# Kernel optimization log

Hardware: AMD Instinct MI355X
Metric: run time of the kernel (lower is better)

## Reference

```python
import jax, jax.numpy as jnp
import numpy as np

N_HEAD = 12

def setup_inputs() -> dict:
    key = jax.random.key(0)
    k1, k2, k3 = jax.random.split(key, 3)
    B, T, C = 2, 4096, 768
    x = jax.random.normal(k1, (B, T, C), dtype=jnp.float32)
    Wqkv = jax.random.normal(k2, (C, 3 * C), dtype=jnp.float32) * (1.0 / np.sqrt(C))
    bqkv = jnp.zeros((3 * C,), dtype=jnp.float32)
    Wout = jax.random.normal(k3, (C, C), dtype=jnp.float32) * (1.0 / np.sqrt(C))
    bout = jnp.zeros((C,), dtype=jnp.float32)
    return {"x": x, "Wqkv": Wqkv, "bqkv": bqkv, "Wout": Wout, "bout": bout}

def reference(x, Wqkv, bqkv, Wout, bout):
    B, T, C = x.shape
    H = N_HEAD
    D = C // H
    qkv = x @ Wqkv + bqkv                       # [B,T,3C]
    qkv = qkv.reshape(B, T, 3, H, D)
    q = qkv[:, :, 0].transpose(0, 2, 1, 3)       # [B,H,T,D]
    k = qkv[:, :, 1].transpose(0, 2, 1, 3)
    v = qkv[:, :, 2].transpose(0, 2, 1, 3)
    att = jnp.einsum('bhqd,bhkd->bhqk', q, k) / jnp.sqrt(jnp.float32(D))
    causal = jnp.tril(jnp.ones((T, T), dtype=bool))
    att = jnp.where(causal[None, None], att, jnp.float32(-jnp.inf))
    att = jax.nn.softmax(att, axis=-1)
    out = jnp.einsum('bhqk,bhkd->bhqd', att, v)  # [B,H,T,D]
    out = out.transpose(0, 2, 1, 3).reshape(B, T, C)
    return out @ Wout + bout
```

## Files before the change

### kernel.cpp

```cpp
#include <hip/hip_runtime.h>
#include <math.h>

#define Bb 2
#define Tt 4096
#define Cc 768
#define Hh 12
#define Dd 64

typedef __attribute__((ext_vector_type(8))) short short8;
typedef __attribute__((ext_vector_type(4))) float f32x4;
typedef __attribute__((ext_vector_type(4))) unsigned short u16x4;

static __device__ __forceinline__ unsigned short f2bf(float f) {
    unsigned u = __float_as_uint(f);
    u += 0x7FFF + ((u >> 16) & 1);
    return (unsigned short)(u >> 16);
}

static __device__ __forceinline__ float ex2(float x) {
    return __builtin_amdgcn_exp2f(x);
}

static __device__ __forceinline__ void gload16(const void* g, void* l) {
    __builtin_amdgcn_global_load_lds(
        (const __attribute__((address_space(1))) unsigned*)g,
        (__attribute__((address_space(3))) unsigned*)l, 16, 0, 0);
}

__global__ __launch_bounds__(256)
void cvt_bf16(const float* __restrict__ in, unsigned short* __restrict__ out, int n8) {
    int i = blockIdx.x * 256 + threadIdx.x;
    if (i >= n8) return;
    float4 a = *(const float4*)(in + (size_t)i * 8);
    float4 b = *(const float4*)(in + (size_t)i * 8 + 4);
    union { short8 v; unsigned short u[8]; } p;
    p.u[0] = f2bf(a.x); p.u[1] = f2bf(a.y); p.u[2] = f2bf(a.z); p.u[3] = f2bf(a.w);
    p.u[4] = f2bf(b.x); p.u[5] = f2bf(b.y); p.u[6] = f2bf(b.z); p.u[7] = f2bf(b.w);
    *(short8*)(out + (size_t)i * 8) = p.v;
}

__global__ __launch_bounds__(256)
void transpose_w(const float* __restrict__ W, unsigned short* __restrict__ Wt,
                 int K, int N) {
    __shared__ __align__(16) unsigned short Tl[64][72];
    int n0 = blockIdx.x * 64, k0 = blockIdx.y * 64;
    int t = threadIdx.x;
    int r = t >> 2, c = (t & 3) * 16;
    const float* wp = W + (size_t)(k0 + r) * N + n0 + c;
    #pragma unroll
    for (int j = 0; j < 16; j += 4) {
        float4 v = *(const float4*)(wp + j);
        Tl[c + j + 0][r] = f2bf(v.x);
        Tl[c + j + 1][r] = f2bf(v.y);
        Tl[c + j + 2][r] = f2bf(v.z);
        Tl[c + j + 3][r] = f2bf(v.w);
    }
    __syncthreads();
    unsigned short* op = Wt + (size_t)(n0 + r) * K + k0 + c;
    *(short8*)op       = *(const short8*)&Tl[r][c];
    *(short8*)(op + 8) = *(const short8*)&Tl[r][c + 8];
}

template<bool BF16OUT>
__global__ __launch_bounds__(256)
void gemm_mfma(const unsigned short* __restrict__ A, const unsigned short* __restrict__ Bt,
               const float* __restrict__ bias, void* __restrict__ Cout,
               int M, int N, int K, int qcols,
               unsigned short* __restrict__ vtb, int voff) {
    union SmemU {
        unsigned short ab[2][128][64];
        unsigned short tv[128][136];
    };
    __shared__ __align__(16) SmemU sh;
    const int tid = threadIdx.x;
    const int wid = tid >> 6, lane = tid & 63;
    const int lr = lane & 15, g = lane >> 4;
    const int wr = wid >> 1, wc = wid & 1;
    const int m0 = blockIdx.y * 128, n0 = blockIdx.x * 128;
    const int srow = lane >> 3;
    const int scol = (lane & 7) * 8;

    f32x4 acc[4][4] = {};

    for (int k0 = 0; k0 < K; k0 += 64) {
        #pragma unroll
        for (int j = 0; j < 4; ++j) {
            int ci = wid * 4 + j;
            int row = ci * 8 + srow;
            gload16(A  + (size_t)(m0 + row) * K + k0 + scol, &sh.ab[0][ci * 8][0]);
            gload16(Bt + (size_t)(n0 + row) * K + k0 + scol, &sh.ab[1][ci * 8][0]);
        }
        __syncthreads();
        #pragma unroll
        for (int ks = 0; ks < 2; ++ks) {
            short8 af[4], bfr[4];
            #pragma unroll
            for (int m = 0; m < 4; ++m)
                af[m] = *(const short8*)&sh.ab[0][wr * 64 + m * 16 + lr][ks * 32 + g * 8];
            #pragma unroll
            for (int n = 0; n < 4; ++n)
                bfr[n] = *(const short8*)&sh.ab[1][wc * 64 + n * 16 + lr][ks * 32 + g * 8];
            #pragma unroll
            for (int m = 0; m < 4; ++m)
                #pragma unroll
                for (int n = 0; n < 4; ++n)
                    acc[m][n] = __builtin_amdgcn_mfma_f32_16x16x32_bf16(
                        af[m], bfr[n], acc[m][n], 0, 0, 0);
        }
        __syncthreads();
    }

    if (vtb != nullptr && n0 >= voff) {
        #pragma unroll
        for (int n = 0; n < 4; ++n) {
            int tcol = wc * 64 + n * 16 + lr;
            float bv = bias[n0 + tcol];
            #pragma unroll
            for (int m = 0; m < 4; ++m) {
                int trow = wr * 64 + m * 16 + g * 4;
                #pragma unroll
                for (int r = 0; r < 4; ++r)
                    sh.tv[tcol][trow + r] = f2bf(acc[m][n][r] + bv);
            }
        }
        __syncthreads();
        const int dlocal = tid >> 1;
        const int th     = (tid & 1) * 64;
        const int colg   = n0 + dlocal;
        const int hd     = (colg - voff) >> 6;
        const int d      = (colg - voff) & 63;
        const int token  = m0 + th;
        const int bq     = token >> 12;
        const int t0     = token & (Tt - 1);
        unsigned short* dst = vtb + ((size_t)(bq * Hh + hd) * Dd + d) * Tt + t0;
        const unsigned short* src = &sh.tv[dlocal][th];
        #pragma unroll
        for (int j = 0; j < 8; ++j)
            *(short8*)(dst + j * 8) = *(const short8*)(src + j * 8);
        return;
    }

    const float qscale = 0.125f * 1.44269504088896340736f;
    #pragma unroll
    for (int n = 0; n < 4; ++n) {
        int coln = n0 + wc * 64 + n * 16 + lr;
        float bv = bias[coln];
        float sc = (coln < qcols) ? qscale : 1.0f;
        #pragma unroll
        for (int m = 0; m < 4; ++m) {
            int rowb = m0 + wr * 64 + m * 16 + g * 4;
            #pragma unroll
            for (int r = 0; r < 4; ++r) {
                float v = (acc[m][n][r] + bv) * sc;
                if (BF16OUT)
                    ((unsigned short*)Cout)[(size_t)(rowb + r) * N + coln] = f2bf(v);
                else
                    ((float*)Cout)[(size_t)(rowb + r) * N + coln] = v;
            }
        }
    }
}

__global__ __launch_bounds__(512)
void attn_mfma(const unsigned short* __restrict__ qkvb,
               const unsigned short* __restrict__ vtb,
               unsigned short* __restrict__ outb) {
    const int nid  = blockIdx.x;
    const int xcd  = nid & 7;
    const int rest = nid >> 3;
    const int P    = rest & 31;
    const int H2   = xcd + 8 * (rest >> 5);
    const int hd   = H2 % Hh;
    const int b    = H2 / Hh;
    const int tid = threadIdx.x;
    const int wid = tid >> 6, lane = tid & 63;
    const int strip = wid & 3, kh = wid >> 2;
    const int lr = lane & 15, g = lane >> 4;
    const int rm7 = lr & 7;
    const size_t rs = 3 * Cc;

    __shared__ __align__(16) unsigned short Ks[2][64 * 64];
    __shared__ __align__(16) unsigned short Vs[2][64 * 64];
    __shared__ __align__(16) float combO[4][64][16];
    __shared__ float combL[4][64];

    const unsigned short* qkvbase = qkvb + (size_t)b * Tt * rs;
    const unsigned short* vbase   = vtb + (size_t)((b * Hh + hd) * Dd) * Tt;

    const int row0 = tid >> 3;
    const int slog = (tid & 7) ^ (row0 & 7);
    const unsigned short* ksrc0 = qkvbase + (size_t)row0 * rs + Cc + hd * Dd + slog * 8;
    const unsigned short* vsrc0 = vbase + (size_t)row0 * Tt + slog * 8;

    const int ntA = 64 - P;
    const int qA  = (63 - P) * 64 + strip * 16 + lr;
    const int qB  = P * 64 + strip * 16 + lr;

    short8 qfA0, qfA1, qfB0, qfB1;
    {
        const unsigned short* qp = qkvbase + (size_t)qA * rs + hd * Dd;
        qfA0 = *(const short8*)(qp + g * 8);
        qfA1 = *(const short8*)(qp + 32 + g * 8);
        qp = qkvbase + (size_t)qB * rs + hd * Dd;
        qfB0 = *(const short8*)(qp + g * 8);
        qfB1 = *(const short8*)(qp + 32 + g * 8);
    }

    auto stage = [&](int buf, int ts) {
        int t = (ts < ntA) ? ts : ts - ntA;
        gload16(ksrc0 + (size_t)t * 64 * rs, &Ks[buf][wid * 512]);
        gload16(vsrc0 + t * 64,              &Vs[buf][wid * 512]);
    };

    stage(0, 0);
    __syncthreads();
    int cur = 0;

    const int laneA = lr + ((g & 1) << 5);
    const int laneB = laneA + 16;
    const int asel  = g >> 1;

    f32x4 o[4];
    #pragma unroll
    for (int dt = 0; dt < 4; ++dt) o[dt] = (f32x4){0.f, 0.f, 0.f, 0.f};
    float lpart = 0.f;
    short8 qf0 = qfA0, qf1 = qfA1;
    int myq = qA;

    auto combine_epilogue = [&]() {
        if (kh) {
            #pragma unroll
            for (int dt = 0; dt < 4; ++dt)
                *(f32x4*)&combO[strip][lane][dt * 4] = o[dt];
            combL[strip][lane] = lpart;
        }
        __syncthreads();
        if (!kh) {
            float l_r = lpart + combL[strip][lane];
            l_r += __shfl_xor(l_r, 16);
            l_r += __shfl_xor(l_r, 32);
            float inv = 1.f / fmaxf(l_r, 1e-37f);
            unsigned short* op = outb + ((size_t)b * Tt + myq) * Cc + hd * Dd + g * 4;
            #pragma unroll
            for (int dt = 0; dt < 4; ++dt) {
                f32x4 t2 = *(const f32x4*)&combO[strip][lane][dt * 4];
                u16x4 w;
                #pragma unroll
                for (int r = 0; r < 4; ++r) w[r] = f2bf((o[dt][r] + t2[r]) * inv);
                *(u16x4*)(op + dt * 16) = w;
            }
        }
        __syncthreads();
    };

    #pragma unroll 1
    for (int ts = 0; ts < 65; ++ts) {
        if (ts + 1 < 65) stage(cur ^ 1, ts + 1);

        const int inA = (ts < ntA) ? 1 : 0;
        const int kbt = inA ? ts : ts - ntA;
        const int nt  = inA ? ntA : (65 - ntA);
        const unsigned short* Kc = &Ks[cur][0];
        const unsigned short* Vc = &Vs[cur][0];

        f32x4 st[2];
        __builtin_amdgcn_s_setprio(1);
        #pragma unroll
        for (int kt = 0; kt < 2; ++kt) {
            int row = kh * 32 + kt * 16 + lr;
            int off0 = row * 64 + (g ^ rm7) * 8;
            short8 kf0 = *(const short8*)&Kc[off0];
            short8 kf1 = *(const short8*)&Kc[off0 ^ 32];
            f32x4 a = (f32x4){0.f, 0.f, 0.f, 0.f};
            a = __builtin_amdgcn_mfma_f32_16x16x32_bf16(kf0, qf0, a, 0, 0, 0);
            a = __builtin_amdgcn_mfma_f32_16x16x32_bf16(kf1, qf1, a, 0, 0, 0);
            st[kt] = a;
        }
        __builtin_amdgcn_s_setprio(0);

        if (kbt == nt - 1) {
            #pragma unroll
            for (int kt = 0; kt < 2; ++kt)
                #pragma unroll
                for (int r = 0; r < 4; ++r)
                    if (kbt * 64 + kh * 32 + kt * 16 + g * 4 + r > myq)
                        st[kt][r] = -1e30f;
        }

        float psum = 0.f;
        #pragma unroll
        for (int kt = 0; kt < 2; ++kt)
            #pragma unroll
            for (int r = 0; r < 4; ++r) {
                float p = ex2(st[kt][r]);
                st[kt][r] = p;
                psum += p;
            }
        lpart += psum;

        unsigned up[2][2];
        #pragma unroll
        for (int kt = 0; kt < 2; ++kt) {
            asm("v_cvt_pk_bf16_f32 %0, %1, %2"
                : "=v"(up[kt][0]) : "v"(st[kt][0]), "v"(st[kt][1]));
            asm("v_cvt_pk_bf16_f32 %0, %1, %2"
                : "=v"(up[kt][1]) : "v"(st[kt][2]), "v"(st[kt][3]));
        }
        {
            unsigned wa0 = __shfl(up[0][0], laneA);
            unsigned wb0 = __shfl(up[1][0], laneA);
            unsigned wa1 = __shfl(up[0][1], laneA);
            unsigned wb1 = __shfl(up[1][1], laneA);
            unsigned wa2 = __shfl(up[0][0], laneB);
            unsigned wb2 = __shfl(up[1][0], laneB);
            unsigned wa3 = __shfl(up[0][1], laneB);
            unsigned wb3 = __shfl(up[1][1], laneB);
            union { unsigned w[4]; short8 v; } pb;
            pb.w[0] = asel ? wb0 : wa0;
            pb.w[1] = asel ? wb1 : wa1;
            pb.w[2] = asel ? wb2 : wa2;
            pb.w[3] = asel ? wb3 : wa3;
            __builtin_amdgcn_s_setprio(1);
            #pragma unroll
            for (int dt = 0; dt < 4; ++dt) {
                int row = dt * 16 + lr;
                int off = row * 64 + (((kh << 2) | g) ^ rm7) * 8;
                short8 vf = *(const short8*)&Vc[off];
                o[dt] = __builtin_amdgcn_mfma_f32_16x16x32_bf16(vf, pb.v, o[dt], 0, 0, 0);
            }
            __builtin_amdgcn_s_setprio(0);
        }

        __syncthreads();
        cur ^= 1;

        if (ts == ntA - 1) {
            combine_epilogue();
            #pragma unroll
            for (int dt = 0; dt < 4; ++dt) o[dt] = (f32x4){0.f, 0.f, 0.f, 0.f};
            lpart = 0.f;
            qf0 = qfB0; qf1 = qfB1;
            myq = qB;
        }
    }

    combine_epilogue();
}

extern "C" void kernel_launch(void* const* d_in, const int* in_sizes, int n_in,
                              void* d_out, int out_size, void* d_ws, size_t ws_size,
                              hipStream_t stream) {
    const float* x    = (const float*)d_in[0];
    const float* Wqkv = (const float*)d_in[1];
    const float* bqkv = (const float*)d_in[2];
    const float* Wout = (const float*)d_in[3];
    const float* bout = (const float*)d_in[4];
    float* out = (float*)d_out;

    const int M = Bb * Tt;
    const int N1 = 3 * Cc;

    char* p = (char*)d_ws;
    unsigned short* qkvb  = (unsigned short*)p; p += (size_t)M * N1 * 2;
    unsigned short* xb    = (unsigned short*)p; p += (size_t)M * Cc * 2;
    unsigned short* wqkvt = (unsigned short*)p; p += (size_t)N1 * Cc * 2;
    unsigned short* woutt = (unsigned short*)p; p += (size_t)Cc * Cc * 2;
    unsigned short* vtb   = (unsigned short*)p; p += (size_t)Bb * Hh * Dd * Tt * 2;
    unsigned short* attb  = (unsigned short*)p; p += (size_t)M * Cc * 2;

    cvt_bf16<<<dim3((M * Cc / 8 + 255) / 256), dim3(256), 0, stream>>>(x, xb, M * Cc / 8);
    transpose_w<<<dim3(N1 / 64, Cc / 64), dim3(256), 0, stream>>>(Wqkv, wqkvt, Cc, N1);
    transpose_w<<<dim3(Cc / 64, Cc / 64), dim3(256), 0, stream>>>(Wout, woutt, Cc, Cc);

    gemm_mfma<true><<<dim3(N1 / 128, M / 128), dim3(256), 0, stream>>>(
        xb, wqkvt, bqkv, qkvb, M, N1, Cc, Cc, vtb, 2 * Cc);

    attn_mfma<<<dim3(32 * Hh * Bb), dim3(512), 0, stream>>>(qkvb, vtb, attb);

    gemm_mfma<false><<<dim3(Cc / 128, M / 128), dim3(256), 0, stream>>>(
        attb, woutt, bout, out, M, Cc, Cc, 0, nullptr, 1 << 30);
}
```

Before: 194.2 us.

## Halve attention block to 4 waves, each handling two 16-row query sub-tiles

The attention kernel now runs 256 threads (4 waves) instead of 8. Each wave processes two 16-row query sub-tiles, so each K and V fragment read from LDS feeds two MFMAs. Each thread issues twice as many staging loads, and per-thread accumulator and register state roughly doubles. The intent is to halve LDS fragment traffic per unit of compute and cut barrier participants, at the cost of fewer waves for latency hiding and higher register pressure.

```diff
diff --git a/kernel.cpp b/kernel.cpp
--- a/kernel.cpp
+++ b/kernel.cpp
@@ -161,7 +161,7 @@
     }
 }
 
-__global__ __launch_bounds__(512)
+__global__ __launch_bounds__(256)
 void attn_mfma(const unsigned short* __restrict__ qkvb,
                const unsigned short* __restrict__ vtb,
                unsigned short* __restrict__ outb) {
@@ -174,42 +174,46 @@
     const int b    = H2 / Hh;
     const int tid = threadIdx.x;
     const int wid = tid >> 6, lane = tid & 63;
-    const int strip = wid & 3, kh = wid >> 2;
+    const int strip = wid & 1, kh = wid >> 1;
     const int lr = lane & 15, g = lane >> 4;
     const int rm7 = lr & 7;
     const size_t rs = 3 * Cc;
 
     __shared__ __align__(16) unsigned short Ks[2][64 * 64];
     __shared__ __align__(16) unsigned short Vs[2][64 * 64];
-    __shared__ __align__(16) float combO[4][64][16];
-    __shared__ float combL[4][64];
+    __shared__ __align__(16) float combO[2][2][64][16];
+    __shared__ float combL[2][2][64];
 
     const unsigned short* qkvbase = qkvb + (size_t)b * Tt * rs;
     const unsigned short* vbase   = vtb + (size_t)((b * Hh + hd) * Dd) * Tt;
 
-    const int row0 = tid >> 3;
-    const int slog = (tid & 7) ^ (row0 & 7);
+    const int srw  = lane >> 3;
+    const int row0 = wid * 8 + srw;
+    const int slog = (lane & 7) ^ (srw & 7);
     const unsigned short* ksrc0 = qkvbase + (size_t)row0 * rs + Cc + hd * Dd + slog * 8;
     const unsigned short* vsrc0 = vbase + (size_t)row0 * Tt + slog * 8;
 
     const int ntA = 64 - P;
-    const int qA  = (63 - P) * 64 + strip * 16 + lr;
-    const int qB  = P * 64 + strip * 16 + lr;
-
-    short8 qfA0, qfA1, qfB0, qfB1;
-    {
-        const unsigned short* qp = qkvbase + (size_t)qA * rs + hd * Dd;
-        qfA0 = *(const short8*)(qp + g * 8);
-        qfA1 = *(const short8*)(qp + 32 + g * 8);
-        qp = qkvbase + (size_t)qB * rs + hd * Dd;
-        qfB0 = *(const short8*)(qp + g * 8);
-        qfB1 = *(const short8*)(qp + 32 + g * 8);
+    const int qA0 = (63 - P) * 64 + strip * 32;
+    const int qB0 = P * 64 + strip * 32;
+
+    short8 qfA[2][2], qfB[2][2];
+    #pragma unroll
+    for (int sub = 0; sub < 2; ++sub) {
+        const unsigned short* qp = qkvbase + (size_t)(qA0 + sub * 16 + lr) * rs + hd * Dd;
+        qfA[sub][0] = *(const short8*)(qp + g * 8);
+        qfA[sub][1] = *(const short8*)(qp + 32 + g * 8);
+        qp = qkvbase + (size_t)(qB0 + sub * 16 + lr) * rs + hd * Dd;
+        qfB[sub][0] = *(const short8*)(qp + g * 8);
+        qfB[sub][1] = *(const short8*)(qp + 32 + g * 8);
     }
 
     auto stage = [&](int buf, int ts) {
         int t = (ts < ntA) ? ts : ts - ntA;
-        gload16(ksrc0 + (size_t)t * 64 * rs, &Ks[buf][wid * 512]);
-        gload16(vsrc0 + t * 64,              &Vs[buf][wid * 512]);
+        gload16(ksrc0 + (size_t)t * 64 * rs,        &Ks[buf][wid * 512]);
+        gload16(ksrc0 + (size_t)(t * 64 + 32) * rs, &Ks[buf][2048 + wid * 512]);
+        gload16(vsrc0 + t * 64,                     &Vs[buf][wid * 512]);
+        gload16(vsrc0 + (size_t)32 * Tt + t * 64,   &Vs[buf][2048 + wid * 512]);
     };
 
     stage(0, 0);
@@ -220,34 +224,48 @@
     const int laneB = laneA + 16;
     const int asel  = g >> 1;
 
-    f32x4 o[4];
+    f32x4 o[2][4];
     #pragma unroll
-    for (int dt = 0; dt < 4; ++dt) o[dt] = (f32x4){0.f, 0.f, 0.f, 0.f};
-    float lpart = 0.f;
-    short8 qf0 = qfA0, qf1 = qfA1;
-    int myq = qA;
+    for (int sub = 0; sub < 2; ++sub)
+        #pragma unroll
+        for (int dt = 0; dt < 4; ++dt) o[sub][dt] = (f32x4){0.f, 0.f, 0.f, 0.f};
+    float lpart[2] = {0.f, 0.f};
+    short8 qf[2][2];
+    #pragma unroll
+    for (int sub = 0; sub < 2; ++sub) {
+        qf[sub][0] = qfA[sub][0]; qf[sub][1] = qfA[sub][1];
+    }
+    int myq0 = qA0 + lr;
 
     auto combine_epilogue = [&]() {
         if (kh) {
             #pragma unroll
-            for (int dt = 0; dt < 4; ++dt)
-                *(f32x4*)&combO[strip][lane][dt * 4] = o[dt];
-            combL[strip][lane] = lpart;
+            for (int sub = 0; sub < 2; ++sub) {
+                #pragma unroll
+                for (int dt = 0; dt < 4; ++dt)
+                    *(f32x4*)&combO[strip][sub][lane][dt * 4] = o[sub][dt];
+                combL[strip][sub][lane] = lpart[sub];
+            }
         }
         __syncthreads();
         if (!kh) {
-            float l_r = lpart + combL[strip][lane];
-            l_r += __shfl_xor(l_r, 16);
-            l_r += __shfl_xor(l_r, 32);
-            float inv = 1.f / fmaxf(l_r, 1e-37f);
-            unsigned short* op = outb + ((size_t)b * Tt + myq) * Cc + hd * Dd + g * 4;
-            #pragma unroll
-            for (int dt = 0; dt < 4; ++dt) {
-                f32x4 t2 = *(const f32x4*)&combO[strip][lane][dt * 4];
-                u16x4 w;
-                #pragma unroll
-                for (int r = 0; r < 4; ++r) w[r] = f2bf((o[dt][r] + t2[r]) * inv);
-                *(u16x4*)(op + dt * 16) = w;
+            #pragma unroll
+            for (int sub = 0; sub < 2; ++sub) {
+                float l_r = lpart[sub] + combL[strip][sub][lane];
+                l_r += __shfl_xor(l_r, 16);
+                l_r += __shfl_xor(l_r, 32);
+                float inv = 1.f / fmaxf(l_r, 1e-37f);
+                unsigned short* op = outb + ((size_t)b * Tt + myq0 + sub * 16) * Cc
+                                     + hd * Dd + g * 4;
+                #pragma unroll
+                for (int dt = 0; dt < 4; ++dt) {
+                    f32x4 t2 = *(const f32x4*)&combO[strip][sub][lane][dt * 4];
+                    u16x4 w;
+                    #pragma unroll
+                    for (int r = 0; r < 4; ++r)
+                        w[r] = f2bf((o[sub][dt][r] + t2[r]) * inv);
+                    *(u16x4*)(op + dt * 16) = w;
+                }
             }
         }
         __syncthreads();
@@ -263,50 +281,63 @@
         const unsigned short* Kc = &Ks[cur][0];
         const unsigned short* Vc = &Vs[cur][0];
 
-        f32x4 st[2];
+        f32x4 st[2][2];
         __builtin_amdgcn_s_setprio(1);
         #pragma unroll
         for (int kt = 0; kt < 2; ++kt) {
-            int row = kh * 32 + kt * 16 + lr;
-            int off0 = row * 64 + (g ^ rm7) * 8;
+            int krow = kh * 32 + kt * 16 + lr;
+            int off0 = krow * 64 + (g ^ rm7) * 8;
             short8 kf0 = *(const short8*)&Kc[off0];
             short8 kf1 = *(const short8*)&Kc[off0 ^ 32];
-            f32x4 a = (f32x4){0.f, 0.f, 0.f, 0.f};
-            a = __builtin_amdgcn_mfma_f32_16x16x32_bf16(kf0, qf0, a, 0, 0, 0);
-            a = __builtin_amdgcn_mfma_f32_16x16x32_bf16(kf1, qf1, a, 0, 0, 0);
-            st[kt] = a;
+            #pragma unroll
+            for (int sub = 0; sub < 2; ++sub) {
+                f32x4 a = (f32x4){0.f, 0.f, 0.f, 0.f};
+                a = __builtin_amdgcn_mfma_f32_16x16x32_bf16(kf0, qf[sub][0], a, 0, 0, 0);
+                a = __builtin_amdgcn_mfma_f32_16x16x32_bf16(kf1, qf[sub][1], a, 0, 0, 0);
+                st[sub][kt] = a;
+            }
         }
         __builtin_amdgcn_s_setprio(0);
 
+        short8 vf[4];
+        #pragma unroll
+        for (int dt = 0; dt < 4; ++dt) {
+            int off = (dt * 16 + lr) * 64 + (((kh << 2) | g) ^ rm7) * 8;
+            vf[dt] = *(const short8*)&Vc[off];
+        }
+
         if (kbt == nt - 1) {
             #pragma unroll
+            for (int sub = 0; sub < 2; ++sub)
+                #pragma unroll
+                for (int kt = 0; kt < 2; ++kt)
+                    #pragma unroll
+                    for (int r = 0; r < 4; ++r)
+                        if (kbt * 64 + kh * 32 + kt * 16 + g * 4 + r > myq0 + sub * 16)
+                            st[sub][kt][r] = -1e30f;
+        }
+
+        #pragma unroll
+        for (int sub = 0; sub < 2; ++sub) {
+            float psum = 0.f;
+            #pragma unroll
             for (int kt = 0; kt < 2; ++kt)
                 #pragma unroll
-                for (int r = 0; r < 4; ++r)
-                    if (kbt * 64 + kh * 32 + kt * 16 + g * 4 + r > myq)
-                        st[kt][r] = -1e30f;
-        }
-
-        float psum = 0.f;
-        #pragma unroll
-        for (int kt = 0; kt < 2; ++kt)
-            #pragma unroll
-            for (int r = 0; r < 4; ++r) {
-                float p = ex2(st[kt][r]);
-                st[kt][r] = p;
-                psum += p;
-            }
-        lpart += psum;
-
-        unsigned up[2][2];
-        #pragma unroll
-        for (int kt = 0; kt < 2; ++kt) {
-            asm("v_cvt_pk_bf16_f32 %0, %1, %2"
-                : "=v"(up[kt][0]) : "v"(st[kt][0]), "v"(st[kt][1]));
-            asm("v_cvt_pk_bf16_f32 %0, %1, %2"
-                : "=v"(up[kt][1]) : "v"(st[kt][2]), "v"(st[kt][3]));
-        }
-        {
+                for (int r = 0; r < 4; ++r) {
+                    float p = ex2(st[sub][kt][r]);
+                    st[sub][kt][r] = p;
+                    psum += p;
+                }
+            lpart[sub] += psum;
+
+            unsigned up[2][2];
+            #pragma unroll
+            for (int kt = 0; kt < 2; ++kt) {
+                asm("v_cvt_pk_bf16_f32 %0, %1, %2"
+                    : "=v"(up[kt][0]) : "v"(st[sub][kt][0]), "v"(st[sub][kt][1]));
+                asm("v_cvt_pk_bf16_f32 %0, %1, %2"
+                    : "=v"(up[kt][1]) : "v"(st[sub][kt][2]), "v"(st[sub][kt][3]));
+            }
             unsigned wa0 = __shfl(up[0][0], laneA);
             unsigned wb0 = __shfl(up[1][0], laneA);
             unsigned wa1 = __shfl(up[0][1], laneA);
@@ -322,12 +353,9 @@
             pb.w[3] = asel ? wb3 : wa3;
             __builtin_amdgcn_s_setprio(1);
             #pragma unroll
-            for (int dt = 0; dt < 4; ++dt) {
-                int row = dt * 16 + lr;
-                int off = row * 64 + (((kh << 2) | g) ^ rm7) * 8;
-                short8 vf = *(const short8*)&Vc[off];
-                o[dt] = __builtin_amdgcn_mfma_f32_16x16x32_bf16(vf, pb.v, o[dt], 0, 0, 0);
-            }
+            for (int dt = 0; dt < 4; ++dt)
+                o[sub][dt] = __builtin_amdgcn_mfma_f32_16x16x32_bf16(
+                    vf[dt], pb.v, o[sub][dt], 0, 0, 0);
             __builtin_amdgcn_s_setprio(0);
         }
 
@@ -337,10 +365,13 @@
         if (ts == ntA - 1) {
             combine_epilogue();
             #pragma unroll
-            for (int dt = 0; dt < 4; ++dt) o[dt] = (f32x4){0.f, 0.f, 0.f, 0.f};
-            lpart = 0.f;
-            qf0 = qfB0; qf1 = qfB1;
-            myq = qB;
+            for (int sub = 0; sub < 2; ++sub) {
+                #pragma unroll
+                for (int dt = 0; dt < 4; ++dt) o[sub][dt] = (f32x4){0.f, 0.f, 0.f, 0.f};
+                lpart[sub] = 0.f;
+                qf[sub][0] = qfB[sub][0]; qf[sub][1] = qfB[sub][1];
+            }
+            myq0 = qB0 + lr;
         }
     }
 
@@ -375,7 +406,7 @@
     gemm_mfma<true><<<dim3(N1 / 128, M / 128), dim3(256), 0, stream>>>(
         xb, wqkvt, bqkv, qkvb, M, N1, Cc, Cc, vtb, 2 * Cc);
 
-    attn_mfma<<<dim3(32 * Hh * Bb), dim3(512), 0, stream>>>(qkvb, vtb, attb);
+    attn_mfma<<<dim3(32 * Hh * Bb), dim3(256), 0, stream>>>(qkvb, vtb, attb);
 
     gemm_mfma<false><<<dim3(Cc / 128, M / 128), dim3(256), 0, stream>>>(
         attb, woutt, bout, out, M, Cc, Cc, 0, nullptr, 1 << 30);
```

Result: slower. 260.6 us (+34.2%).

## Pre-pack K and V into MFMA fragment order and load directly from global

Applied to the files above, without the earlier changes.

The QKV GEMM epilogue now writes K and V tiles in a per-head, per-64-token fragment-packed layout, and Q into its own buffer. The attention kernel drops the LDS double-buffered staging and its per-tile __syncthreads, loading K/V fragments straight from global memory as contiguous 16-byte per-lane reads. This removes LDS traffic and block-wide barriers in the inner loop and frees LDS to allow more resident blocks. The cost is exposed global/L2 latency without explicit prefetching, plus duplicated K/V reads across the waves that share a tile.

```diff
diff --git a/kernel.cpp b/kernel.cpp
--- a/kernel.cpp
+++ b/kernel.cpp
@@ -65,8 +65,8 @@
 __global__ __launch_bounds__(256)
 void gemm_mfma(const unsigned short* __restrict__ A, const unsigned short* __restrict__ Bt,
                const float* __restrict__ bias, void* __restrict__ Cout,
-               int M, int N, int K, int qcols,
-               unsigned short* __restrict__ vtb, int voff) {
+               int M, int N, int K,
+               unsigned short* __restrict__ kpk, unsigned short* __restrict__ vpk) {
     union SmemU {
         unsigned short ab[2][128][64];
         unsigned short tv[128][136];
@@ -110,7 +110,7 @@
         __syncthreads();
     }
 
-    if (vtb != nullptr && n0 >= voff) {
+    if (BF16OUT && vpk != nullptr && n0 >= 2 * Cc) {
         #pragma unroll
         for (int n = 0; n < 4; ++n) {
             int tcol = wc * 64 + n * 16 + lr;
@@ -126,17 +126,55 @@
         __syncthreads();
         const int dlocal = tid >> 1;
         const int th     = (tid & 1) * 64;
-        const int colg   = n0 + dlocal;
-        const int hd     = (colg - voff) >> 6;
-        const int d      = (colg - voff) & 63;
+        const int hd     = ((n0 - 2 * Cc) >> 6) + (dlocal >> 6);
+        const int dl     = dlocal & 63;
+        const int dt     = dl >> 4, lrv = dl & 15;
         const int token  = m0 + th;
         const int bq     = token >> 12;
-        const int t0     = token & (Tt - 1);
-        unsigned short* dst = vtb + ((size_t)(bq * Hh + hd) * Dd + d) * Tt + t0;
-        const unsigned short* src = &sh.tv[dlocal][th];
-        #pragma unroll
-        for (int j = 0; j < 8; ++j)
-            *(short8*)(dst + j * 8) = *(const short8*)(src + j * 8);
+        const int tile   = (token & (Tt - 1)) >> 6;
+        unsigned short* tb = vpk + (size_t)((bq * Hh + hd) * 64 + tile) * 4096;
+        #pragma unroll
+        for (int cj = 0; cj < 8; ++cj) {
+            int khv = cj >> 2, gv = cj & 3;
+            unsigned short* dst = tb + (dt * 2 + khv) * 512 + (gv * 16 + lrv) * 8;
+            *(short8*)dst = *(const short8*)&sh.tv[dlocal][th + cj * 8];
+        }
+        return;
+    }
+
+    if (BF16OUT && kpk != nullptr && n0 >= Cc) {
+        #pragma unroll
+        for (int n = 0; n < 4; ++n) {
+            int tcol = wc * 64 + n * 16 + lr;
+            float bv = bias[n0 + tcol];
+            #pragma unroll
+            for (int m = 0; m < 4; ++m) {
+                int trow = wr * 64 + m * 16 + g * 4;
+                #pragma unroll
+                for (int r = 0; r < 4; ++r)
+                    sh.tv[trow + r][tcol] = f2bf(acc[m][n][r] + bv);
+            }
+        }
+        __syncthreads();
+        #pragma unroll
+        for (int c = 0; c < 8; ++c) {
+            int s = tid + 256 * c;
+            int ln = s & 63;
+            int f  = (s >> 6) & 7;
+            int hh = (s >> 9) & 1;
+            int sub = s >> 10;
+            int khk = f >> 2, ktk = (f >> 1) & 1, ksk = f & 1;
+            int gk = ln >> 4, lrk = ln & 15;
+            int tokl = sub * 64 + khk * 32 + ktk * 16 + lrk;
+            int dl   = hh * 64 + ksk * 32 + gk * 8;
+            int token = m0 + sub * 64;
+            int bq    = token >> 12;
+            int tile  = (token & (Tt - 1)) >> 6;
+            int hd    = ((n0 - Cc) >> 6) + hh;
+            unsigned short* dst = kpk + (size_t)((bq * Hh + hd) * 64 + tile) * 4096
+                                  + f * 512 + ln * 8;
+            *(short8*)dst = *(const short8*)&sh.tv[tokl][dl];
+        }
         return;
     }
 
@@ -145,15 +183,15 @@
     for (int n = 0; n < 4; ++n) {
         int coln = n0 + wc * 64 + n * 16 + lr;
         float bv = bias[coln];
-        float sc = (coln < qcols) ? qscale : 1.0f;
         #pragma unroll
         for (int m = 0; m < 4; ++m) {
             int rowb = m0 + wr * 64 + m * 16 + g * 4;
             #pragma unroll
             for (int r = 0; r < 4; ++r) {
-                float v = (acc[m][n][r] + bv) * sc;
+                float v = acc[m][n][r] + bv;
                 if (BF16OUT)
-                    ((unsigned short*)Cout)[(size_t)(rowb + r) * N + coln] = f2bf(v);
+                    ((unsigned short*)Cout)[(size_t)(rowb + r) * Cc + coln] =
+                        f2bf(v * qscale);
                 else
                     ((float*)Cout)[(size_t)(rowb + r) * N + coln] = v;
             }
@@ -161,9 +199,10 @@
     }
 }
 
-__global__ __launch_bounds__(512)
-void attn_mfma(const unsigned short* __restrict__ qkvb,
-               const unsigned short* __restrict__ vtb,
+__global__ __launch_bounds__(512, 6)
+void attn_mfma(const unsigned short* __restrict__ qb,
+               const unsigned short* __restrict__ kpk,
+               const unsigned short* __restrict__ vpk,
                unsigned short* __restrict__ outb) {
     const int nid  = blockIdx.x;
     const int xcd  = nid & 7;
@@ -176,45 +215,27 @@
     const int wid = tid >> 6, lane = tid & 63;
     const int strip = wid & 3, kh = wid >> 2;
     const int lr = lane & 15, g = lane >> 4;
-    const int rm7 = lr & 7;
-    const size_t rs = 3 * Cc;
-
-    __shared__ __align__(16) unsigned short Ks[2][64 * 64];
-    __shared__ __align__(16) unsigned short Vs[2][64 * 64];
+
     __shared__ __align__(16) float combO[4][64][16];
     __shared__ float combL[4][64];
 
-    const unsigned short* qkvbase = qkvb + (size_t)b * Tt * rs;
-    const unsigned short* vbase   = vtb + (size_t)((b * Hh + hd) * Dd) * Tt;
-
-    const int row0 = tid >> 3;
-    const int slog = (tid & 7) ^ (row0 & 7);
-    const unsigned short* ksrc0 = qkvbase + (size_t)row0 * rs + Cc + hd * Dd + slog * 8;
-    const unsigned short* vsrc0 = vbase + (size_t)row0 * Tt + slog * 8;
+    const unsigned short* qbase = qb + (size_t)b * Tt * Cc;
+    const unsigned short* kbase = kpk + (size_t)((b * Hh + hd) * 64) * 4096;
+    const unsigned short* vbase = vpk + (size_t)((b * Hh + hd) * 64) * 4096;
 
     const int ntA = 64 - P;
     const int qA  = (63 - P) * 64 + strip * 16 + lr;
     const int qB  = P * 64 + strip * 16 + lr;
 
-    short8 qfA0, qfA1, qfB0, qfB1;
+    const int kfo = kh * 2048 + lane * 8;
+    const int vfo = kh * 512 + lane * 8;
+
+    short8 qf0, qf1;
     {
-        const unsigned short* qp = qkvbase + (size_t)qA * rs + hd * Dd;
-        qfA0 = *(const short8*)(qp + g * 8);
-        qfA1 = *(const short8*)(qp + 32 + g * 8);
-        qp = qkvbase + (size_t)qB * rs + hd * Dd;
-        qfB0 = *(const short8*)(qp + g * 8);
-        qfB1 = *(const short8*)(qp + 32 + g * 8);
-    }
-
-    auto stage = [&](int buf, int ts) {
-        int t = (ts < ntA) ? ts : ts - ntA;
-        gload16(ksrc0 + (size_t)t * 64 * rs, &Ks[buf][wid * 512]);
-        gload16(vsrc0 + t * 64,              &Vs[buf][wid * 512]);
-    };
-
-    stage(0, 0);
-    __syncthreads();
-    int cur = 0;
+        const unsigned short* qp = qbase + (size_t)qA * Cc + hd * Dd;
+        qf0 = *(const short8*)(qp + g * 8);
+        qf1 = *(const short8*)(qp + 32 + g * 8);
+    }
 
     const int laneA = lr + ((g & 1) << 5);
     const int laneB = laneA + 16;
@@ -224,7 +245,6 @@
     #pragma unroll
     for (int dt = 0; dt < 4; ++dt) o[dt] = (f32x4){0.f, 0.f, 0.f, 0.f};
     float lpart = 0.f;
-    short8 qf0 = qfA0, qf1 = qfA1;
     int myq = qA;
 
     auto combine_epilogue = [&]() {
@@ -255,28 +275,32 @@
 
     #pragma unroll 1
     for (int ts = 0; ts < 65; ++ts) {
-        if (ts + 1 < 65) stage(cur ^ 1, ts + 1);
-
         const int inA = (ts < ntA) ? 1 : 0;
         const int kbt = inA ? ts : ts - ntA;
         const int nt  = inA ? ntA : (65 - ntA);
-        const unsigned short* Kc = &Ks[cur][0];
-        const unsigned short* Vc = &Vs[cur][0];
-
+        const unsigned short* kt_ = kbase + (size_t)kbt * 4096;
+        const unsigned short* vt_ = vbase + (size_t)kbt * 4096;
+
+        short8 kf00 = *(const short8*)(kt_ + kfo);
+        short8 kf01 = *(const short8*)(kt_ + kfo + 512);
+        short8 kf10 = *(const short8*)(kt_ + kfo + 1024);
+        short8 kf11 = *(const short8*)(kt_ + kfo + 1536);
         f32x4 st[2];
-        __builtin_amdgcn_s_setprio(1);
-        #pragma unroll
-        for (int kt = 0; kt < 2; ++kt) {
-            int row = kh * 32 + kt * 16 + lr;
-            int off0 = row * 64 + (g ^ rm7) * 8;
-            short8 kf0 = *(const short8*)&Kc[off0];
-            short8 kf1 = *(const short8*)&Kc[off0 ^ 32];
+        {
             f32x4 a = (f32x4){0.f, 0.f, 0.f, 0.f};
-            a = __builtin_amdgcn_mfma_f32_16x16x32_bf16(kf0, qf0, a, 0, 0, 0);
-            a = __builtin_amdgcn_mfma_f32_16x16x32_bf16(kf1, qf1, a, 0, 0, 0);
-            st[kt] = a;
-        }
-        __builtin_amdgcn_s_setprio(0);
+            a = __builtin_amdgcn_mfma_f32_16x16x32_bf16(kf00, qf0, a, 0, 0, 0);
+            a = __builtin_amdgcn_mfma_f32_16x16x32_bf16(kf01, qf1, a, 0, 0, 0);
+            st[0] = a;
+            a = (f32x4){0.f, 0.f, 0.f, 0.f};
+            a = __builtin_amdgcn_mfma_f32_16x16x32_bf16(kf10, qf0, a, 0, 0, 0);
+            a = __builtin_amdgcn_mfma_f32_16x16x32_bf16(kf11, qf1, a, 0, 0, 0);
+            st[1] = a;
+        }
+
+        short8 vf0 = *(const short8*)(vt_ + vfo);
+        short8 vf1 = *(const short8*)(vt_ + vfo + 1024);
+        short8 vf2 = *(const short8*)(vt_ + vfo + 2048);
+        short8 vf3 = *(const short8*)(vt_ + vfo + 3072);
 
         if (kbt == nt - 1) {
             #pragma unroll
@@ -306,40 +330,33 @@
             asm("v_cvt_pk_bf16_f32 %0, %1, %2"
                 : "=v"(up[kt][1]) : "v"(st[kt][2]), "v"(st[kt][3]));
         }
-        {
-            unsigned wa0 = __shfl(up[0][0], laneA);
-            unsigned wb0 = __shfl(up[1][0], laneA);
-            unsigned wa1 = __shfl(up[0][1], laneA);
-            unsigned wb1 = __shfl(up[1][1], laneA);
-            unsigned wa2 = __shfl(up[0][0], laneB);
-            unsigned wb2 = __shfl(up[1][0], laneB);
-            unsigned wa3 = __shfl(up[0][1], laneB);
-            unsigned wb3 = __shfl(up[1][1], laneB);
-            union { unsigned w[4]; short8 v; } pb;
-            pb.w[0] = asel ? wb0 : wa0;
-            pb.w[1] = asel ? wb1 : wa1;
-            pb.w[2] = asel ? wb2 : wa2;
-            pb.w[3] = asel ? wb3 : wa3;
-            __builtin_amdgcn_s_setprio(1);
-            #pragma unroll
-            for (int dt = 0; dt < 4; ++dt) {
-                int row = dt * 16 + lr;
-                int off = row * 64 + (((kh << 2) | g) ^ rm7) * 8;
-                short8 vf = *(const short8*)&Vc[off];
-                o[dt] = __builtin_amdgcn_mfma_f32_16x16x32_bf16(vf, pb.v, o[dt], 0, 0, 0);
-            }
-            __builtin_amdgcn_s_setprio(0);
-        }
-
-        __syncthreads();
-        cur ^= 1;
+        unsigned wa0 = __shfl(up[0][0], laneA);
+        unsigned wb0 = __shfl(up[1][0], laneA);
+        unsigned wa1 = __shfl(up[0][1], laneA);
+        unsigned wb1 = __shfl(up[1][1], laneA);
+        unsigned wa2 = __shfl(up[0][0], laneB);
+        unsigned wb2 = __shfl(up[1][0], laneB);
+        unsigned wa3 = __shfl(up[0][1], laneB);
+        unsigned wb3 = __shfl(up[1][1], laneB);
+        union { unsigned w[4]; short8 v; } pb;
+        pb.w[0] = asel ? wb0 : wa0;
+        pb.w[1] = asel ? wb1 : wa1;
+        pb.w[2] = asel ? wb2 : wa2;
+        pb.w[3] = asel ? wb3 : wa3;
+
+        o[0] = __builtin_amdgcn_mfma_f32_16x16x32_bf16(vf0, pb.v, o[0], 0, 0, 0);
+        o[1] = __builtin_amdgcn_mfma_f32_16x16x32_bf16(vf1, pb.v, o[1], 0, 0, 0);
+        o[2] = __builtin_amdgcn_mfma_f32_16x16x32_bf16(vf2, pb.v, o[2], 0, 0, 0);
+        o[3] = __builtin_amdgcn_mfma_f32_16x16x32_bf16(vf3, pb.v, o[3], 0, 0, 0);
 
         if (ts == ntA - 1) {
             combine_epilogue();
             #pragma unroll
             for (int dt = 0; dt < 4; ++dt) o[dt] = (f32x4){0.f, 0.f, 0.f, 0.f};
             lpart = 0.f;
-            qf0 = qfB0; qf1 = qfB1;
+            const unsigned short* qp = qbase + (size_t)qB * Cc + hd * Dd;
+            qf0 = *(const short8*)(qp + g * 8);
+            qf1 = *(const short8*)(qp + 32 + g * 8);
             myq = qB;
         }
     }
@@ -361,11 +378,12 @@
     const int N1 = 3 * Cc;
 
     char* p = (char*)d_ws;
-    unsigned short* qkvb  = (unsigned short*)p; p += (size_t)M * N1 * 2;
+    unsigned short* qbuf  = (unsigned short*)p; p += (size_t)M * Cc * 2;
     unsigned short* xb    = (unsigned short*)p; p += (size_t)M * Cc * 2;
     unsigned short* wqkvt = (unsigned short*)p; p += (size_t)N1 * Cc * 2;
     unsigned short* woutt = (unsigned short*)p; p += (size_t)Cc * Cc * 2;
-    unsigned short* vtb   = (unsigned short*)p; p += (size_t)Bb * Hh * Dd * Tt * 2;
+    unsigned short* kpk   = (unsigned short*)p; p += (size_t)Bb * Hh * 64 * 4096 * 2;
+    unsigned short* vpk   = (unsigned short*)p; p += (size_t)Bb * Hh * 64 * 4096 * 2;
     unsigned short* attb  = (unsigned short*)p; p += (size_t)M * Cc * 2;
 
     cvt_bf16<<<dim3((M * Cc / 8 + 255) / 256), dim3(256), 0, stream>>>(x, xb, M * Cc / 8);
@@ -373,10 +391,10 @@
     transpose_w<<<dim3(Cc / 64, Cc / 64), dim3(256), 0, stream>>>(Wout, woutt, Cc, Cc);
 
     gemm_mfma<true><<<dim3(N1 / 128, M / 128), dim3(256), 0, stream>>>(
-        xb, wqkvt, bqkv, qkvb, M, N1, Cc, Cc, vtb, 2 * Cc);
-
-    attn_mfma<<<dim3(32 * Hh * Bb), dim3(512), 0, stream>>>(qkvb, vtb, attb);
+        xb, wqkvt, bqkv, qbuf, M, N1, Cc, kpk, vpk);
+
+    attn_mfma<<<dim3(32 * Hh * Bb), dim3(512), 0, stream>>>(qbuf, kpk, vpk, attb);
 
     gemm_mfma<false><<<dim3(Cc / 128, M / 128), dim3(256), 0, stream>>>(
-        attb, woutt, bout, out, M, Cc, Cc, 0, nullptr, 1 << 30);
-}
+        attb, woutt, bout, out, M, Cc, Cc, nullptr, nullptr);
+}
```

Result: slower. 199.6 us (+2.8%).
